# Kernel tuning notes

Hardware: AMD Instinct MI355X
Metric: run time of the kernel (lower is better)

## Reference

```python
import jax, jax.numpy as jnp
import numpy as np
from jax import lax

B, H, W = 8, 64, 64
D_IN, D_OUT, HEADS = 288, 576, 8
WIN, QS = 16, 2
MLP_H, BOT, NEXP = 4 * D_OUT, 32, 2
HEAD_DIM = D_OUT // HEADS


def _ln(x, g, b, eps=1e-6):
    m = jnp.mean(x, axis=-1, keepdims=True)
    v = jnp.var(x, axis=-1, keepdims=True)
    return (x - m) * lax.rsqrt(v + eps) * g + b


def _max_pool2(x):  # NHWC 2x2 max pool, stride 2
    return lax.reduce_window(x, -jnp.inf, lax.max, (1, 2, 2, 1), (1, 2, 2, 1), 'VALID')


def setup_inputs():
    key = jax.random.key(0)
    ks = iter(jax.random.split(key, 16))
    s = 0.02
    p = {}
    p['rgb'] = jax.random.normal(next(ks), (B, H, W, D_IN), jnp.float32)
    p['depth'] = jax.random.normal(next(ks), (B, H, W, D_IN), jnp.float32)
    p['norm1_g'] = jnp.ones((D_IN,), jnp.float32)
    p['norm1_b'] = jnp.zeros((D_IN,), jnp.float32)
    p['proj_w'] = jax.random.normal(next(ks), (D_IN, D_OUT), jnp.float32) * s
    p['proj_b'] = jnp.zeros((D_OUT,), jnp.float32)
    p['qkv_w'] = jax.random.normal(next(ks), (D_IN, 3 * D_OUT), jnp.float32) * s
    p['qkv_b'] = jnp.zeros((3 * D_OUT,), jnp.float32)
    p['attn_proj_w'] = jax.random.normal(next(ks), (D_OUT, D_OUT), jnp.float32) * s
    p['attn_proj_b'] = jnp.zeros((D_OUT,), jnp.float32)
    p['norm2_g'] = jnp.ones((D_OUT,), jnp.float32)
    p['norm2_b'] = jnp.zeros((D_OUT,), jnp.float32)
    p['mlp_w1'] = jax.random.normal(next(ks), (D_OUT, MLP_H), jnp.float32) * s
    p['mlp_b1'] = jnp.zeros((MLP_H,), jnp.float32)
    p['mlp_w2'] = jax.random.normal(next(ks), (MLP_H, D_OUT), jnp.float32) * s
    p['mlp_b2'] = jnp.zeros((D_OUT,), jnp.float32)
    # per-stream (rgb=0, depth=1) MoE adapters: 2 experts, bottleneck 32
    p['ad_gate_w'] = jax.random.normal(next(ks), (2, D_OUT, NEXP), jnp.float32) * s
    p['ad_gate_b'] = jnp.zeros((2, NEXP), jnp.float32)
    p['ad_down_w'] = jax.random.normal(next(ks), (2, NEXP, D_OUT, BOT), jnp.float32) * s
    p['ad_down_b'] = jnp.zeros((2, NEXP, BOT), jnp.float32)
    p['ad_up_w'] = jax.random.normal(next(ks), (2, NEXP, BOT, D_OUT), jnp.float32) * s
    p['ad_up_b'] = jnp.zeros((2, NEXP, D_OUT), jnp.float32)
    return p


def reference(rgb, depth, norm1_g, norm1_b, proj_w, proj_b, qkv_w, qkv_b,
              attn_proj_w, attn_proj_b, norm2_g, norm2_b,
              mlp_w1, mlp_b1, mlp_w2, mlp_b2,
              ad_gate_w, ad_gate_b, ad_down_w, ad_down_b, ad_up_w, ad_up_b):
    nW = H // WIN  # 4 windows per side (64 divisible by 16, no padding)
    w2 = WIN // QS  # pooled window side = 8

    def adapter(x, si):
        gate = jax.nn.softmax(x @ ad_gate_w[si] + ad_gate_b[si], axis=-1)  # [B,h,w,E]
        h = jax.nn.gelu(jnp.einsum('bhwd,edr->bhwer', x, ad_down_w[si]) + ad_down_b[si])
        y = jnp.einsum('bhwer,erd->bhwed', h, ad_up_w[si]) + ad_up_b[si]
        return 0.5 * jnp.sum(gate[..., None] * y, axis=-2)

    def stream(x, si):
        xn = _ln(x, norm1_g, norm1_b)
        # dim changes -> shortcut = do_pool(proj(norm1(x)))
        shortcut = _max_pool2(xn @ proj_w + proj_b)  # [B,32,32,576]
        xw = xn.reshape(B, nW, WIN, nW, WIN, D_IN).transpose(0, 1, 3, 2, 4, 5)
        xw = xw.reshape(B * nW * nW, WIN, WIN, D_IN)
        Bw = xw.shape[0]
        qkv = (xw.reshape(Bw, WIN * WIN, D_IN) @ qkv_w + qkv_b)
        qkv = qkv.reshape(Bw, WIN * WIN, 3, HEADS, HEAD_DIM)
        q, k, v = qkv[:, :, 0], qkv[:, :, 1], qkv[:, :, 2]
        # q-pool (2x2 max) inside each window
        q = _max_pool2(q.reshape(Bw, WIN, WIN, D_OUT)).reshape(Bw, w2 * w2, HEADS, HEAD_DIM)
        scale = 1.0 / np.sqrt(HEAD_DIM).astype(np.float32)
        attn = jax.nn.softmax(jnp.einsum('bqhd,bkhd->bhqk', q, k) * scale, axis=-1)
        o = jnp.einsum('bhqk,bkhd->bqhd', attn, v).reshape(Bw, w2, w2, D_OUT)
        o = o @ attn_proj_w + attn_proj_b
        # unpartition with pooled window size into 32x32
        o = o.reshape(B, nW, nW, w2, w2, D_OUT).transpose(0, 1, 3, 2, 4, 5)
        o = o.reshape(B, nW * w2, nW * w2, D_OUT)
        x = shortcut + o
        h = _ln(x, norm2_g, norm2_b)
        mlp = jax.nn.gelu(h @ mlp_w1 + mlp_b1) @ mlp_w2 + mlp_b2
        return x + mlp + adapter(x, si)

    return jnp.stack([stream(rgb, 0), stream(depth, 1)])  # [2,B,32,32,576]
```

## Files before the change

### kernel.cpp

```cpp
#include <hip/hip_runtime.h>
#include <cstdint>
#include <math.h>
#include <type_traits>

typedef __bf16 bf16_t;
typedef __bf16 bf16x8 __attribute__((ext_vector_type(8)));
typedef float f32x4 __attribute__((ext_vector_type(4)));
typedef uint32_t u32x4 __attribute__((ext_vector_type(4)));
typedef uint32_t u32x2 __attribute__((ext_vector_type(2)));

#define DI __device__ __forceinline__

DI float bflo(uint32_t u){ return __builtin_bit_cast(float, (uint32_t)(u << 16)); }
DI float bfhi(uint32_t u){ return __builtin_bit_cast(float, (uint32_t)(u & 0xffff0000u)); }
DI uint16_t f2bf(float f){ bf16_t h = (bf16_t)f; return __builtin_bit_cast(uint16_t, h); }
DI uint32_t pk2(float a, float b){ return (uint32_t)f2bf(a) | ((uint32_t)f2bf(b) << 16); }
DI float geluf(float x){
  float t = x * x;
  float p = fmaf(t, 0.0356774081f, 0.7978845608f);
  float e = __expf(-2.0f * x * p);
  return x * __builtin_amdgcn_rcpf(1.0f + e);
}

#if defined(__has_builtin)
#if __has_builtin(__builtin_amdgcn_global_load_lds)
#define USE_GLLDS 1
#endif
#endif

#if USE_GLLDS
DI void gload_lds16(const void* g, void* l){
  __builtin_amdgcn_global_load_lds((__attribute__((address_space(1))) void*)g,
                                   (__attribute__((address_space(3))) void*)l, 16, 0, 0);
}
#endif

__global__ __launch_bounds__(256) void wprep_k(
    const float* __restrict__ proj_w, const float* __restrict__ qkv_w,
    const float* __restrict__ ap_w, const float* __restrict__ w1,
    const float* __restrict__ proj_b, const float* __restrict__ qkv_b,
    uint16_t* __restrict__ pqT, uint16_t* __restrict__ kvT,
    uint16_t* __restrict__ aT, uint16_t* __restrict__ m1T, float* __restrict__ pqB)
{
  const int y = blockIdx.y;
  const int idx = blockIdx.x * 256 + threadIdx.x;
  if (y == 5){
    if (idx < 1152) pqB[idx] = (idx < 576) ? proj_b[idx] : qkv_b[idx - 576];
    return;
  }
  const float* W; uint16_t* Wt; int K, N, Np, ldw, c0;
  switch (y){
    case 0: W = proj_w; Wt = pqT;                      K = 288; N = 576;  Np = 576;  ldw = 576;  c0 = 0;   break;
    case 1: W = qkv_w;  Wt = pqT + (size_t)576 * 288;  K = 288; N = 576;  Np = 576;  ldw = 1728; c0 = 0;   break;
    case 2: W = qkv_w;  Wt = kvT;                      K = 288; N = 1152; Np = 1152; ldw = 1728; c0 = 576; break;
    case 3: W = ap_w;   Wt = aT;                       K = 576; N = 576;  Np = 640;  ldw = 576;  c0 = 0;   break;
    default:W = w1;     Wt = m1T;                      K = 576; N = 2304; Np = 2304; ldw = 2304; c0 = 0;   break;
  }
  if (idx >= Np * K) return;
  int n = idx / K, k = idx - n * K;
  float v = (n < N) ? W[(size_t)k * ldw + c0 + n] : 0.0f;
  Wt[idx] = f2bf(v);
}

__global__ __launch_bounds__(256) void mk_m2te_k(const float* __restrict__ w2,
    const float* __restrict__ uw, const float* __restrict__ ub, uint16_t* __restrict__ m2Te)
{
  int idx = blockIdx.x * 256 + threadIdx.x;
  if (idx >= 2 * 640 * 2400) return;
  int si = idx / (640 * 2400);
  int rem = idx - si * 640 * 2400;
  int n = rem / 2400, k = rem - n * 2400;
  float v = 0.0f;
  if (n < 576){
    if (k < 2304) v = w2[(size_t)k * 576 + n];
    else if (k < 2368){
      int e = (k - 2304) >> 5, r = (k - 2304) & 31;
      v = uw[((size_t)(si * 2 + e) * 32 + r) * 576 + n];
    } else if (k < 2370){
      v = ub[(size_t)(si * 2 + (k - 2368)) * 576 + n];
    }
  }
  m2Te[idx] = f2bf(v);
}

__global__ __launch_bounds__(256) void mk_adt_k(const float* __restrict__ dwn, const float* __restrict__ gw,
    const float* __restrict__ dbn, const float* __restrict__ gb,
    uint16_t* __restrict__ adT, float* __restrict__ adB)
{
  int idx = blockIdx.x * 256 + threadIdx.x;
  if (idx >= 2 * 128 * 576) return;
  int si = idx / (128 * 576);
  int rem = idx - si * 128 * 576;
  int n = rem / 576, k = rem - n * 576;
  float v = 0.0f;
  if (n < 64){
    int e = n >> 5, r = n & 31;
    v = dwn[((size_t)(si * 2 + e) * 576 + k) * 32 + r];
  } else if (n < 66){
    v = gw[(size_t)si * 1152 + k * 2 + (n - 64)];
  }
  adT[idx] = f2bf(v);
  if (k == 0){
    float bv = 0.0f;
    if (n < 64) bv = dbn[si * 64 + (n >> 5) * 32 + (n & 31)];
    else if (n < 66) bv = gb[si * 2 + (n - 64)];
    adB[si * 128 + n] = bv;
  }
}

template<typename TIN>
__global__ __launch_bounds__(256) void ln_k(const TIN* __restrict__ inA, const TIN* __restrict__ inB,
                                            const int rowsA, const int D,
                                            const float* __restrict__ g, const float* __restrict__ bb,
                                            uint16_t* __restrict__ outp)
{
  const int token = blockIdx.x * 4 + (threadIdx.x >> 6);
  const int lane = threadIdx.x & 63;
  const TIN* in = (token < rowsA) ? (inA + (size_t)token * D) : (inB + (size_t)(token - rowsA) * D);
  const int nf4 = D >> 2;
  f32x4 v[3];
  float s = 0.f, sq = 0.f;
#pragma unroll
  for (int i = 0; i < 3; ++i){
    const int c = lane + 64 * i;
    if (c < nf4){
      if constexpr (std::is_same<TIN, float>::value){
        v[i] = *(const f32x4*)(in + 4 * c);
      } else {
        u32x2 u = *(const u32x2*)((const uint16_t*)in + 4 * c);
        v[i][0] = bflo(u[0]); v[i][1] = bfhi(u[0]);
        v[i][2] = bflo(u[1]); v[i][3] = bfhi(u[1]);
      }
#pragma unroll
      for (int e = 0; e < 4; ++e){ s += v[i][e]; sq += v[i][e] * v[i][e]; }
    }
  }
#pragma unroll
  for (int off = 32; off; off >>= 1){
    s  += __shfl_xor(s, off);
    sq += __shfl_xor(sq, off);
  }
  const float mean = s / (float)D;
  const float var = sq / (float)D - mean * mean;
  const float inv = rsqrtf(var + 1e-6f);
  uint16_t* orow = outp + (size_t)token * D;
#pragma unroll
  for (int i = 0; i < 3; ++i){
    const int c = lane + 64 * i;
    if (c < nf4){
      float f0 = (v[i][0] - mean) * inv * g[4*c+0] + bb[4*c+0];
      float f1 = (v[i][1] - mean) * inv * g[4*c+1] + bb[4*c+1];
      float f2 = (v[i][2] - mean) * inv * g[4*c+2] + bb[4*c+2];
      float f3 = (v[i][3] - mean) * inv * g[4*c+3] + bb[4*c+3];
      u32x2 pk; pk[0] = pk2(f0, f1); pk[1] = pk2(f2, f3);
      *(u32x2*)(orow + 4 * c) = pk;
    }
  }
}

template<int BM, int KK>
DI void gemm_core(const uint16_t* __restrict__ A, const uint16_t* __restrict__ Bt,
                  char* smem, const int tid, f32x4 (*acc)[4])
{
  constexpr int MI = BM / 32;
  constexpr int ABUF = BM * 64;
  constexpr int nt = KK >> 5;
  char* A0 = smem;
  char* A1 = smem + ABUF;
  char* B0 = smem + 2 * ABUF;
  char* B1 = smem + 2 * ABUF + 8192;
  const int lane = tid & 63;
  const int wid = tid >> 6;
  const int wm = (wid >> 1) * (BM / 2);
  const int wn = (wid & 1) * 64;
  const int r15 = lane & 15, kh = lane >> 4;
  const int rA0 = tid >> 2, c16 = tid & 3;
  const int kS = ((c16 ^ ((rA0 >> 1) & 3)) << 3);

  auto stage = [&](char* Ad, char* Bd, int t){
    const uint16_t* ga0 = A + (size_t)rA0 * KK + t * 32 + kS;
    const uint16_t* gb0 = Bt + (size_t)rA0 * KK + t * 32 + kS;
    const uint16_t* gb1 = Bt + (size_t)(rA0 + 64) * KK + t * 32 + kS;
#if USE_GLLDS
    gload_lds16(ga0, Ad + tid * 16);
    gload_lds16(gb0, Bd + tid * 16);
    gload_lds16(gb1, Bd + tid * 16 + 4096);
    if constexpr (BM == 128){
      const uint16_t* ga1 = A + (size_t)(rA0 + 64) * KK + t * 32 + kS;
      gload_lds16(ga1, Ad + tid * 16 + 4096);
    }
#else
    *(u32x4*)(Ad + tid * 16)        = *(const u32x4*)ga0;
    *(u32x4*)(Bd + tid * 16)        = *(const u32x4*)gb0;
    *(u32x4*)(Bd + tid * 16 + 4096) = *(const u32x4*)gb1;
    if constexpr (BM == 128){
      const uint16_t* ga1 = A + (size_t)(rA0 + 64) * KK + t * 32 + kS;
      *(u32x4*)(Ad + tid * 16 + 4096) = *(const u32x4*)ga1;
    }
#endif
  };

  stage(A0, B0, 0);
  __syncthreads();
  for (int t = 0; t < nt; ++t){
    char* Ac = (t & 1) ? A1 : A0;
    char* Bc = (t & 1) ? B1 : B0;
    if (t + 1 < nt) stage((t & 1) ? A0 : A1, (t & 1) ? B0 : B1, t + 1);
    bf16x8 af[MI], bfv[4];
#pragma unroll
    for (int i = 0; i < MI; ++i){
      int rowA = wm + i * 16 + r15;
      af[i] = *(const bf16x8*)(Ac + rowA * 64 + ((kh ^ ((rowA >> 1) & 3)) << 4));
    }
#pragma unroll
    for (int j = 0; j < 4; ++j){
      int rowB = wn + j * 16 + r15;
      bfv[j] = *(const bf16x8*)(Bc + rowB * 64 + ((kh ^ ((rowB >> 1) & 3)) << 4));
    }
#pragma unroll
    for (int i = 0; i < MI; ++i)
#pragma unroll
      for (int j = 0; j < 4; ++j)
        acc[i][j] = __builtin_amdgcn_mfma_f32_16x16x32_bf16(af[i], bfv[j], acc[i][j], 0, 0, 0);
    __syncthreads();
  }
}

__global__ __launch_bounds__(256) void gemm_pkv_k(
    const uint16_t* __restrict__ xn, const uint16_t* __restrict__ pqT, const uint16_t* __restrict__ kvT,
    const float* __restrict__ pqB, const float* __restrict__ kvB,
    uint16_t* __restrict__ sc, uint16_t* __restrict__ qp,
    uint16_t* __restrict__ kb, uint16_t* __restrict__ vt)
{
  __shared__ __align__(16) char smem[34816];
  const int tid = threadIdx.x;
  const int m0 = blockIdx.x * 128;
  const int y = blockIdx.y;
  const bool pool = (y < 9);
  const int n0 = pool ? y * 128 : (y - 9) * 128;
  const uint16_t* Bt = (pool ? pqT : kvT) + (size_t)n0 * 288;
  f32x4 acc[4][4] = {};
  gemm_core<128, 288>(xn + (size_t)m0 * 288, Bt, smem, tid, acc);

  const int lane = tid & 63, wid = tid >> 6;
  const int wm = (wid >> 1) * 64, wn = (wid & 1) * 64;
  const int r15 = lane & 15, kh = lane >> 4;

  if (pool){
    uint16_t* Cp = (uint16_t*)smem;
#pragma unroll
    for (int i = 0; i < 4; ++i)
#pragma unroll
      for (int j = 0; j < 4; ++j)
#pragma unroll
        for (int tt = 0; tt < 4; ++tt){
          int rr2 = wm + i * 16 + kh * 4 + tt;
          int cc = wn + j * 16 + r15;
          Cp[rr2 * 136 + cc] = f2bf(acc[i][j][tt]);
        }
    __syncthreads();
    const int orow0 = m0 >> 2;
#pragma unroll
    for (int e2 = 0; e2 < 16; ++e2){
      int idx = tid + 256 * e2;
      int X = idx >> 7, c = idx & 127;
      int gn = n0 + c;
      float v0 = bflo(Cp[(2 * X) * 136 + c]);
      float v1 = bflo(Cp[(2 * X + 1) * 136 + c]);
      float v2 = bflo(Cp[(64 + 2 * X) * 136 + c]);
      float v3 = bflo(Cp[(65 + 2 * X) * 136 + c]);
      float v = fmaxf(fmaxf(v0, v1), fmaxf(v2, v3)) + pqB[gn];
      if (gn < 576)
        sc[(size_t)(orow0 + X) * 576 + gn] = f2bf(v);
      else
        qp[(size_t)(orow0 + X) * 576 + (gn - 576)] = f2bf(v);
    }
  } else {
    int coln[4]; float bcol[4];
#pragma unroll
    for (int j = 0; j < 4; ++j){
      coln[j] = n0 + wn + j * 16 + r15;
      bcol[j] = kvB[coln[j]];
    }
#pragma unroll
    for (int i = 0; i < 4; ++i)
#pragma unroll
      for (int tt = 0; tt < 4; ++tt){
        const int gm = m0 + wm + i * 16 + kh * 4 + tt;
#pragma unroll
        for (int j = 0; j < 4; ++j){
          float v = acc[i][j][tt] + bcol[j];
          int n = coln[j];
          if (n < 576){
            kb[(size_t)gm * 576 + n] = f2bf(v);
          } else {
            int d = n - 576;
            int hh = d / 72, dd = d - hh * 72;
            int bimg = gm >> 12, yy = (gm >> 6) & 63, xx = gm & 63;
            int w = bimg * 16 + (yy >> 4) * 4 + (xx >> 4);
            int kl = (yy & 15) * 16 + (xx & 15);
            vt[((size_t)(w * 8 + hh) * 80 + dd) * 256 + kl] = f2bf(v);
          }
        }
      }
  }
}

__global__ __launch_bounds__(256) void gemm_add1_k(
    const uint16_t* __restrict__ ob, const uint16_t* __restrict__ aT, const float* __restrict__ bias,
    const uint16_t* __restrict__ sc, uint16_t* __restrict__ x2b)
{
  __shared__ __align__(16) char smem[32768];
  const int tid = threadIdx.x;
  const int m0 = blockIdx.x * 128;
  const int n0 = blockIdx.y * 128;
  f32x4 acc[4][4] = {};
  gemm_core<128, 576>(ob + (size_t)m0 * 576, aT + (size_t)n0 * 576, smem, tid, acc);

  const int lane = tid & 63, wid = tid >> 6;
  const int wm = (wid >> 1) * 64, wn = (wid & 1) * 64;
  const int r15 = lane & 15, kh = lane >> 4;
  int coln[4]; float bcol[4];
#pragma unroll
  for (int j = 0; j < 4; ++j){
    coln[j] = n0 + wn + j * 16 + r15;
    bcol[j] = (coln[j] < 576) ? bias[coln[j]] : 0.0f;
  }
#pragma unroll
  for (int i = 0; i < 4; ++i)
#pragma unroll
    for (int tt = 0; tt < 4; ++tt){
      const int gm = m0 + wm + i * 16 + kh * 4 + tt;
      const size_t ro = (size_t)gm * 576;
#pragma unroll
      for (int j = 0; j < 4; ++j){
        if (coln[j] < 576){
          float v = acc[i][j][tt] + bcol[j] + bflo(sc[ro + coln[j]]);
          x2b[ro + coln[j]] = f2bf(v);
        }
      }
    }
}

__global__ __launch_bounds__(256) void gemm_upad_k(
    const uint16_t* __restrict__ hb, const uint16_t* __restrict__ x2b,
    const uint16_t* __restrict__ m1T, const uint16_t* __restrict__ adT,
    const float* __restrict__ b1, const float* __restrict__ adB,
    uint16_t* __restrict__ mlpA)
{
  __shared__ __align__(16) char smem[32768];
  const int tid = threadIdx.x;
  const int m0 = blockIdx.x * 128;
  const int y = blockIdx.y;
  const bool up = (y < 18);
  const int si = m0 >> 13;
  const int n0 = up ? y * 128 : 0;
  const uint16_t* A = (up ? hb : x2b) + (size_t)m0 * 576;
  const uint16_t* Bt = up ? (m1T + (size_t)n0 * 576) : (adT + (size_t)si * 128 * 576);
  f32x4 acc[4][4] = {};
  gemm_core<128, 576>(A, Bt, smem, tid, acc);

  const int lane = tid & 63, wid = tid >> 6;
  const int wm = (wid >> 1) * 64, wn = (wid & 1) * 64;
  const int r15 = lane & 15, kh = lane >> 4;

  if (up){
#pragma unroll
    for (int i = 0; i < 4; ++i)
#pragma unroll
      for (int tt = 0; tt < 4; ++tt){
        const int gm = m0 + wm + i * 16 + kh * 4 + tt;
#pragma unroll
        for (int j = 0; j < 4; ++j){
          int c = n0 + wn + j * 16 + r15;
          float v = acc[i][j][tt] + b1[c];
          mlpA[(size_t)gm * 2400 + c] = f2bf(geluf(v));
        }
      }
  } else {
    const float* adBp = adB + si * 128;
    float* gl = (float*)smem;
#pragma unroll
    for (int i = 0; i < 4; ++i)
#pragma unroll
      for (int j = 0; j < 4; ++j){
        int c = wn + j * 16 + r15;
        if (c == 64 || c == 65){
#pragma unroll
          for (int tt = 0; tt < 4; ++tt){
            int rr2 = wm + i * 16 + kh * 4 + tt;
            gl[rr2 * 2 + (c - 64)] = acc[i][j][tt] + adBp[c];
          }
        }
      }
    __syncthreads();
#pragma unroll
    for (int i = 0; i < 4; ++i)
#pragma unroll
      for (int tt = 0; tt < 4; ++tt){
        int rr2 = wm + i * 16 + kh * 4 + tt;
        int gm = m0 + rr2;
        float l0 = gl[rr2 * 2], l1 = gl[rr2 * 2 + 1];
        float mx = fmaxf(l0, l1);
        float e0 = __expf(l0 - mx), e1 = __expf(l1 - mx);
        float inv = 0.5f / (e0 + e1);
#pragma unroll
        for (int j = 0; j < 4; ++j){
          int c = wn + j * 16 + r15;
          if (c < 96){
            float val;
            if (c < 64){
              float g = ((c >> 5) == 0 ? e0 : e1) * inv;
              val = g * geluf(acc[i][j][tt] + adBp[c]);
            } else if (c == 64) val = e0 * inv;
            else if (c == 65) val = e1 * inv;
            else val = 0.0f;
            mlpA[(size_t)gm * 2400 + 2304 + c] = f2bf(val);
          }
        }
      }
  }
}

__global__ __launch_bounds__(256) void gemm_addf_k(
    const uint16_t* __restrict__ mlpA, const uint16_t* __restrict__ m2Te, const float* __restrict__ bias,
    const uint16_t* __restrict__ x2b, float* __restrict__ outf)
{
  __shared__ __align__(16) char smem[32768];
  const int tid = threadIdx.x;
  const int m0 = blockIdx.x * 128;
  const int n0 = blockIdx.y * 128;
  const int si = m0 >> 13;
  f32x4 acc[4][4] = {};
  gemm_core<128, 2400>(mlpA + (size_t)m0 * 2400, m2Te + (size_t)si * 640 * 2400 + (size_t)n0 * 2400,
                       smem, tid, acc);

  const int lane = tid & 63, wid = tid >> 6;
  const int wm = (wid >> 1) * 64, wn = (wid & 1) * 64;
  const int r15 = lane & 15, kh = lane >> 4;
  int coln[4]; float bcol[4];
#pragma unroll
  for (int j = 0; j < 4; ++j){
    coln[j] = n0 + wn + j * 16 + r15;
    bcol[j] = (coln[j] < 576) ? bias[coln[j]] : 0.0f;
  }
#pragma unroll
  for (int i = 0; i < 4; ++i)
#pragma unroll
    for (int tt = 0; tt < 4; ++tt){
      const int gm = m0 + wm + i * 16 + kh * 4 + tt;
      const size_t ro = (size_t)gm * 576;
#pragma unroll
      for (int j = 0; j < 4; ++j){
        if (coln[j] < 576){
          float v = acc[i][j][tt] + bcol[j] + bflo(x2b[ro + coln[j]]);
          outf[ro + coln[j]] = v;
        }
      }
    }
}

__global__ __launch_bounds__(128) void attn_mfma_k(
    const uint16_t* __restrict__ qp,
    const uint16_t* __restrict__ kb,
    const uint16_t* __restrict__ vt,
    uint16_t* __restrict__ o)
{
  __shared__ float comb[64][88];
  const int tid = threadIdx.x;
  const int wave = tid >> 6;
  const int lane = tid & 63;
  const int r15 = lane & 15;
  const int kh = lane >> 4;
  const int bid = blockIdx.x;
  const int h = bid & 7;
  const int w = bid >> 3;
  const int b = w >> 4;
  const int wy = (w >> 2) & 3;
  const int wx = w & 3;

  const u32x4 ZU = {0, 0, 0, 0};
  const bf16x8 Z8 = __builtin_bit_cast(bf16x8, ZU);
  const float scale = 0.11785113019775793f;

  bf16x8 qf[4][3];
  int qrow[4];
#pragma unroll
  for (int j = 0; j < 4; ++j){
    int q = j * 16 + r15;
    int y = wy * 8 + (q >> 3), x = wx * 8 + (q & 7);
    qrow[j] = b * 1024 + y * 32 + x;
    const uint16_t* qpr = qp + (size_t)qrow[j] * 576 + h * 72;
    qf[j][0] = *(const bf16x8*)(qpr + kh * 8);
    qf[j][1] = *(const bf16x8*)(qpr + 32 + kh * 8);
    qf[j][2] = (kh == 0) ? *(const bf16x8*)(qpr + 64) : Z8;
  }

  float m[4], l[4];
#pragma unroll
  for (int j = 0; j < 4; ++j){ m[j] = -INFINITY; l[j] = 0.0f; }
  f32x4 acco[5][4] = {};
  const size_t vtbase = (size_t)(w * 8 + h) * 80 * 256;

#pragma unroll
  for (int t2 = 0; t2 < 2; ++t2){
    const int t = wave * 2 + t2;
    f32x4 accs[4][4] = {};
#pragma unroll
    for (int i = 0; i < 4; ++i){
      const uint16_t* kr = kb + (size_t)(b * 4096 + (wy * 16 + t * 4 + i) * 64 + wx * 16 + r15) * 576 + h * 72;
      bf16x8 kf0 = *(const bf16x8*)(kr + kh * 8);
      bf16x8 kf1 = *(const bf16x8*)(kr + 32 + kh * 8);
      bf16x8 kf2 = (kh == 0) ? *(const bf16x8*)(kr + 64) : Z8;
#pragma unroll
      for (int j = 0; j < 4; ++j){
        accs[i][j] = __builtin_amdgcn_mfma_f32_16x16x32_bf16(kf0, qf[j][0], accs[i][j], 0, 0, 0);
        accs[i][j] = __builtin_amdgcn_mfma_f32_16x16x32_bf16(kf1, qf[j][1], accs[i][j], 0, 0, 0);
        accs[i][j] = __builtin_amdgcn_mfma_f32_16x16x32_bf16(kf2, qf[j][2], accs[i][j], 0, 0, 0);
      }
    }
#pragma unroll
    for (int j = 0; j < 4; ++j){
      float mx = -INFINITY;
#pragma unroll
      for (int i = 0; i < 4; ++i)
#pragma unroll
        for (int tt = 0; tt < 4; ++tt){
          float sv = accs[i][j][tt] * scale;
          accs[i][j][tt] = sv;
          mx = fmaxf(mx, sv);
        }
      mx = fmaxf(mx, __shfl_xor(mx, 16));
      mx = fmaxf(mx, __shfl_xor(mx, 32));
      float nm = fmaxf(m[j], mx);
      float f = __expf(m[j] - nm);
      m[j] = nm;
      l[j] *= f;
#pragma unroll
      for (int i2 = 0; i2 < 5; ++i2) acco[i2][j] *= f;
      float ls = 0.0f;
#pragma unroll
      for (int i = 0; i < 4; ++i)
#pragma unroll
        for (int tt = 0; tt < 4; ++tt){
          float p = __expf(accs[i][j][tt] - nm);
          accs[i][j][tt] = p;
          ls += p;
        }
      ls += __shfl_xor(ls, 16);
      ls += __shfl_xor(ls, 32);
      l[j] += ls;
    }
    uint32_t pw[4][4][2];
#pragma unroll
    for (int i = 0; i < 4; ++i)
#pragma unroll
      for (int j = 0; j < 4; ++j){
        pw[i][j][0] = pk2(accs[i][j][0], accs[i][j][1]);
        pw[i][j][1] = pk2(accs[i][j][2], accs[i][j][3]);
      }
#pragma unroll
    for (int ks = 0; ks < 2; ++ks){
      bf16x8 pb[4];
#pragma unroll
      for (int j = 0; j < 4; ++j){
        u32x4 u = {pw[2 * ks][j][0], pw[2 * ks][j][1], pw[2 * ks + 1][j][0], pw[2 * ks + 1][j][1]};
        pb[j] = __builtin_bit_cast(bf16x8, u);
      }
#pragma unroll
      for (int i2 = 0; i2 < 5; ++i2){
        const uint16_t* vr = vt + vtbase + (size_t)(i2 * 16 + r15) * 256 + t * 64 + ks * 32 + kh * 4;
        u32x2 lo = *(const u32x2*)(vr);
        u32x2 hi = *(const u32x2*)(vr + 16);
        u32x4 av = {lo[0], lo[1], hi[0], hi[1]};
        bf16x8 va = __builtin_bit_cast(bf16x8, av);
#pragma unroll
        for (int j = 0; j < 4; ++j)
          acco[i2][j] = __builtin_amdgcn_mfma_f32_16x16x32_bf16(va, pb[j], acco[i2][j], 0, 0, 0);
      }
    }
  }

  if (wave == 1){
#pragma unroll
    for (int j = 0; j < 4; ++j){ comb[lane][j] = m[j]; comb[lane][4 + j] = l[j]; }
#pragma unroll
    for (int i2 = 0; i2 < 5; ++i2)
#pragma unroll
      for (int j = 0; j < 4; ++j)
#pragma unroll
        for (int tt = 0; tt < 4; ++tt)
          comb[lane][8 + (i2 * 4 + j) * 4 + tt] = acco[i2][j][tt];
  }
  __syncthreads();
  if (wave == 0){
    float fs0[4], fs1[4];
#pragma unroll
    for (int j = 0; j < 4; ++j){
      float m1v = comb[lane][j], l1v = comb[lane][4 + j];
      float nm = fmaxf(m[j], m1v);
      fs0[j] = __expf(m[j] - nm);
      fs1[j] = __expf(m1v - nm);
      l[j] = l[j] * fs0[j] + l1v * fs1[j];
    }
#pragma unroll
    for (int j = 0; j < 4; ++j){
      float inv = 1.0f / l[j];
      uint16_t* orow = o + (size_t)qrow[j] * 576 + h * 72;
#pragma unroll
      for (int i2 = 0; i2 < 5; ++i2){
        const int d0 = i2 * 16 + kh * 4;
        if (d0 < 72){
          float ov[4];
#pragma unroll
          for (int tt = 0; tt < 4; ++tt)
            ov[tt] = (acco[i2][j][tt] * fs0[j] + comb[lane][8 + (i2 * 4 + j) * 4 + tt] * fs1[j]) * inv;
          u32x2 pk; pk[0] = pk2(ov[0], ov[1]); pk[1] = pk2(ov[2], ov[3]);
          *(u32x2*)(orow + d0) = pk;
        }
      }
    }
  }
}

extern "C" void kernel_launch(void* const* d_in, const int* in_sizes, int n_in,
                              void* d_out, int out_size, void* d_ws, size_t ws_size,
                              hipStream_t stream)
{
  (void)in_sizes; (void)n_in; (void)out_size; (void)ws_size;
  const float* rgb    = (const float*)d_in[0];
  const float* depth  = (const float*)d_in[1];
  const float* n1g    = (const float*)d_in[2];
  const float* n1b    = (const float*)d_in[3];
  const float* proj_w = (const float*)d_in[4];
  const float* proj_b = (const float*)d_in[5];
  const float* qkv_w  = (const float*)d_in[6];
  const float* qkv_b  = (const float*)d_in[7];
  const float* ap_w   = (const float*)d_in[8];
  const float* ap_b   = (const float*)d_in[9];
  const float* n2g    = (const float*)d_in[10];
  const float* n2b    = (const float*)d_in[11];
  const float* w1     = (const float*)d_in[12];
  const float* b1     = (const float*)d_in[13];
  const float* w2     = (const float*)d_in[14];
  const float* b2     = (const float*)d_in[15];
  const float* gw     = (const float*)d_in[16];
  const float* gb     = (const float*)d_in[17];
  const float* dwn    = (const float*)d_in[18];
  const float* dbn    = (const float*)d_in[19];
  const float* uw     = (const float*)d_in[20];
  const float* ub     = (const float*)d_in[21];

  char* ws = (char*)d_ws;
  size_t off = 0;
  auto alloc = [&](size_t bytes){ size_t o = off; off += (bytes + 255) & ~(size_t)255; return o; };

  uint16_t* pqT   = (uint16_t*)(ws + alloc((size_t)1152 * 288 * 2));
  float*    pqB   = (float*)(ws + alloc((size_t)1152 * 4));
  uint16_t* kvT   = (uint16_t*)(ws + alloc((size_t)1152 * 288 * 2));
  uint16_t* aT    = (uint16_t*)(ws + alloc((size_t)640 * 576 * 2));
  uint16_t* m1T   = (uint16_t*)(ws + alloc((size_t)2304 * 576 * 2));
  uint16_t* m2Te  = (uint16_t*)(ws + alloc((size_t)2 * 640 * 2400 * 2));
  uint16_t* adT   = (uint16_t*)(ws + alloc((size_t)2 * 128 * 576 * 2));
  float*    adB   = (float*)(ws + alloc((size_t)2 * 128 * 4));
  uint16_t* xn2  = (uint16_t*)(ws + alloc((size_t)65536 * 288 * 2));
  uint16_t* sc2  = (uint16_t*)(ws + alloc((size_t)16384 * 576 * 2));
  size_t oQP = alloc((size_t)16384 * 576 * 2);
  uint16_t* qp2  = (uint16_t*)(ws + oQP);
  uint16_t* x2b  = (uint16_t*)(ws + oQP);
  uint16_t* kb   = (uint16_t*)(ws + alloc((size_t)32768 * 576 * 2));
  size_t oVT = alloc((size_t)16384 * 2400 * 2);
  uint16_t* vt   = (uint16_t*)(ws + oVT);
  uint16_t* mlpA = (uint16_t*)(ws + oVT);
  size_t oOB = alloc((size_t)16384 * 576 * 2);
  uint16_t* ob2  = (uint16_t*)(ws + oOB);
  uint16_t* hb2  = (uint16_t*)(ws + oOB);

  wprep_k<<<dim3(5184, 6), 256, 0, stream>>>(proj_w, qkv_w, ap_w, w1, proj_b, qkv_b,
                                             pqT, kvT, aT, m1T, pqB);
  mk_m2te_k<<<(2 * 640 * 2400 + 255) / 256, 256, 0, stream>>>(w2, uw, ub, m2Te);
  mk_adt_k<<<(2 * 128 * 576 + 255) / 256, 256, 0, stream>>>(dwn, gw, dbn, gb, adT, adB);

  ln_k<float><<<16384, 256, 0, stream>>>(rgb, depth, 32768, 288, n1g, n1b, xn2);

  for (int si = 0; si < 2; ++si){
    const size_t half = (size_t)si * 8192 * 576;

    gemm_pkv_k<<<dim3(256, 18), 256, 0, stream>>>(xn2 + (size_t)si * 32768 * 288, pqT, kvT,
                                                  pqB, qkv_b + 576,
                                                  sc2 + half, qp2 + half, kb, vt);

    attn_mfma_k<<<1024, 128, 0, stream>>>(qp2 + half, kb, vt, ob2 + half);
  }

  gemm_add1_k<<<dim3(128, 5), 256, 0, stream>>>(ob2, aT, ap_b, sc2, x2b);

  ln_k<uint16_t><<<4096, 256, 0, stream>>>(x2b, x2b, 16384, 576, n2g, n2b, hb2);

  gemm_upad_k<<<dim3(128, 19), 256, 0, stream>>>(hb2, x2b, m1T, adT, b1, adB, mlpA);

  gemm_addf_k<<<dim3(128, 5), 256, 0, stream>>>(mlpA, m2Te, b2, x2b, (float*)d_out);
}
```

Baseline: 556.7 us.

## Merge weight-prep kernels and swap GEMM grid order for A-tile reuse

Folds the two separate weight-conversion kernels (m2Te and adapter transposes) into the main wprep kernel as extra grid rows, cutting two launches. It also swaps the grid dimensions of all four GEMM kernels, so the N-tile index runs fastest and consecutive blocks share the same M-row A tile. The intent is better L2 reuse of the large activation operands, with less launch overhead as a side benefit. The merged prep grid is much larger (12000x8), and most blocks in the smaller rows exit immediately.

```diff
diff --git a/kernel.cpp b/kernel.cpp
--- a/kernel.cpp
+++ b/kernel.cpp
@@ -39,13 +39,56 @@
     const float* __restrict__ proj_w, const float* __restrict__ qkv_w,
     const float* __restrict__ ap_w, const float* __restrict__ w1,
     const float* __restrict__ proj_b, const float* __restrict__ qkv_b,
+    const float* __restrict__ w2, const float* __restrict__ uw, const float* __restrict__ ub,
+    const float* __restrict__ dwn, const float* __restrict__ gw,
+    const float* __restrict__ dbn, const float* __restrict__ gb,
     uint16_t* __restrict__ pqT, uint16_t* __restrict__ kvT,
-    uint16_t* __restrict__ aT, uint16_t* __restrict__ m1T, float* __restrict__ pqB)
+    uint16_t* __restrict__ aT, uint16_t* __restrict__ m1T, float* __restrict__ pqB,
+    uint16_t* __restrict__ m2Te, uint16_t* __restrict__ adT, float* __restrict__ adB)
 {
   const int y = blockIdx.y;
   const int idx = blockIdx.x * 256 + threadIdx.x;
   if (y == 5){
     if (idx < 1152) pqB[idx] = (idx < 576) ? proj_b[idx] : qkv_b[idx - 576];
+    return;
+  }
+  if (y == 6){
+    if (idx >= 2 * 640 * 2400) return;
+    int si = idx / (640 * 2400);
+    int rem = idx - si * 640 * 2400;
+    int n = rem / 2400, k = rem - n * 2400;
+    float v = 0.0f;
+    if (n < 576){
+      if (k < 2304) v = w2[(size_t)k * 576 + n];
+      else if (k < 2368){
+        int e = (k - 2304) >> 5, r = (k - 2304) & 31;
+        v = uw[((size_t)(si * 2 + e) * 32 + r) * 576 + n];
+      } else if (k < 2370){
+        v = ub[(size_t)(si * 2 + (k - 2368)) * 576 + n];
+      }
+    }
+    m2Te[idx] = f2bf(v);
+    return;
+  }
+  if (y == 7){
+    if (idx >= 2 * 128 * 576) return;
+    int si = idx / (128 * 576);
+    int rem = idx - si * 128 * 576;
+    int n = rem / 576, k = rem - n * 576;
+    float v = 0.0f;
+    if (n < 64){
+      int e = n >> 5, r = n & 31;
+      v = dwn[((size_t)(si * 2 + e) * 576 + k) * 32 + r];
+    } else if (n < 66){
+      v = gw[(size_t)si * 1152 + k * 2 + (n - 64)];
+    }
+    adT[idx] = f2bf(v);
+    if (k == 0){
+      float bv = 0.0f;
+      if (n < 64) bv = dbn[si * 64 + (n >> 5) * 32 + (n & 31)];
+      else if (n < 66) bv = gb[si * 2 + (n - 64)];
+      adB[si * 128 + n] = bv;
+    }
     return;
   }
   const float* W; uint16_t* Wt; int K, N, Np, ldw, c0;
@@ -60,52 +103,6 @@
   int n = idx / K, k = idx - n * K;
   float v = (n < N) ? W[(size_t)k * ldw + c0 + n] : 0.0f;
   Wt[idx] = f2bf(v);
-}
-
-__global__ __launch_bounds__(256) void mk_m2te_k(const float* __restrict__ w2,
-    const float* __restrict__ uw, const float* __restrict__ ub, uint16_t* __restrict__ m2Te)
-{
-  int idx = blockIdx.x * 256 + threadIdx.x;
-  if (idx >= 2 * 640 * 2400) return;
-  int si = idx / (640 * 2400);
-  int rem = idx - si * 640 * 2400;
-  int n = rem / 2400, k = rem - n * 2400;
-  float v = 0.0f;
-  if (n < 576){
-    if (k < 2304) v = w2[(size_t)k * 576 + n];
-    else if (k < 2368){
-      int e = (k - 2304) >> 5, r = (k - 2304) & 31;
-      v = uw[((size_t)(si * 2 + e) * 32 + r) * 576 + n];
-    } else if (k < 2370){
-      v = ub[(size_t)(si * 2 + (k - 2368)) * 576 + n];
-    }
-  }
-  m2Te[idx] = f2bf(v);
-}
-
-__global__ __launch_bounds__(256) void mk_adt_k(const float* __restrict__ dwn, const float* __restrict__ gw,
-    const float* __restrict__ dbn, const float* __restrict__ gb,
-    uint16_t* __restrict__ adT, float* __restrict__ adB)
-{
-  int idx = blockIdx.x * 256 + threadIdx.x;
-  if (idx >= 2 * 128 * 576) return;
-  int si = idx / (128 * 576);
-  int rem = idx - si * 128 * 576;
-  int n = rem / 576, k = rem - n * 576;
-  float v = 0.0f;
-  if (n < 64){
-    int e = n >> 5, r = n & 31;
-    v = dwn[((size_t)(si * 2 + e) * 576 + k) * 32 + r];
-  } else if (n < 66){
-    v = gw[(size_t)si * 1152 + k * 2 + (n - 64)];
-  }
-  adT[idx] = f2bf(v);
-  if (k == 0){
-    float bv = 0.0f;
-    if (n < 64) bv = dbn[si * 64 + (n >> 5) * 32 + (n & 31)];
-    else if (n < 66) bv = gb[si * 2 + (n - 64)];
-    adB[si * 128 + n] = bv;
-  }
 }
 
 template<typename TIN>
@@ -234,8 +231,8 @@
 {
   __shared__ __align__(16) char smem[34816];
   const int tid = threadIdx.x;
-  const int m0 = blockIdx.x * 128;
-  const int y = blockIdx.y;
+  const int m0 = blockIdx.y * 128;
+  const int y = blockIdx.x;
   const bool pool = (y < 9);
   const int n0 = pool ? y * 128 : (y - 9) * 128;
   const uint16_t* Bt = (pool ? pqT : kvT) + (size_t)n0 * 288;
@@ -312,8 +309,8 @@
 {
   __shared__ __align__(16) char smem[32768];
   const int tid = threadIdx.x;
-  const int m0 = blockIdx.x * 128;
-  const int n0 = blockIdx.y * 128;
+  const int m0 = blockIdx.y * 128;
+  const int n0 = blockIdx.x * 128;
   f32x4 acc[4][4] = {};
   gemm_core<128, 576>(ob + (size_t)m0 * 576, aT + (size_t)n0 * 576, smem, tid, acc);
 
@@ -350,8 +347,8 @@
 {
   __shared__ __align__(16) char smem[32768];
   const int tid = threadIdx.x;
-  const int m0 = blockIdx.x * 128;
-  const int y = blockIdx.y;
+  const int m0 = blockIdx.y * 128;
+  const int y = blockIdx.x;
   const bool up = (y < 18);
   const int si = m0 >> 13;
   const int n0 = up ? y * 128 : 0;
@@ -428,8 +425,8 @@
 {
   __shared__ __align__(16) char smem[32768];
   const int tid = threadIdx.x;
-  const int m0 = blockIdx.x * 128;
-  const int n0 = blockIdx.y * 128;
+  const int m0 = blockIdx.y * 128;
+  const int n0 = blockIdx.x * 128;
   const int si = m0 >> 13;
   f32x4 acc[4][4] = {};
   gemm_core<128, 2400>(mlpA + (size_t)m0 * 2400, m2Te + (size_t)si * 640 * 2400 + (size_t)n0 * 2400,
@@ -676,28 +673,27 @@
   uint16_t* ob2  = (uint16_t*)(ws + oOB);
   uint16_t* hb2  = (uint16_t*)(ws + oOB);
 
-  wprep_k<<<dim3(5184, 6), 256, 0, stream>>>(proj_w, qkv_w, ap_w, w1, proj_b, qkv_b,
-                                             pqT, kvT, aT, m1T, pqB);
-  mk_m2te_k<<<(2 * 640 * 2400 + 255) / 256, 256, 0, stream>>>(w2, uw, ub, m2Te);
-  mk_adt_k<<<(2 * 128 * 576 + 255) / 256, 256, 0, stream>>>(dwn, gw, dbn, gb, adT, adB);
+  wprep_k<<<dim3(12000, 8), 256, 0, stream>>>(proj_w, qkv_w, ap_w, w1, proj_b, qkv_b,
+                                              w2, uw, ub, dwn, gw, dbn, gb,
+                                              pqT, kvT, aT, m1T, pqB, m2Te, adT, adB);
 
   ln_k<float><<<16384, 256, 0, stream>>>(rgb, depth, 32768, 288, n1g, n1b, xn2);
 
   for (int si = 0; si < 2; ++si){
     const size_t half = (size_t)si * 8192 * 576;
 
-    gemm_pkv_k<<<dim3(256, 18), 256, 0, stream>>>(xn2 + (size_t)si * 32768 * 288, pqT, kvT,
+    gemm_pkv_k<<<dim3(18, 256), 256, 0, stream>>>(xn2 + (size_t)si * 32768 * 288, pqT, kvT,
                                                   pqB, qkv_b + 576,
                                                   sc2 + half, qp2 + half, kb, vt);
 
     attn_mfma_k<<<1024, 128, 0, stream>>>(qp2 + half, kb, vt, ob2 + half);
   }
 
-  gemm_add1_k<<<dim3(128, 5), 256, 0, stream>>>(ob2, aT, ap_b, sc2, x2b);
+  gemm_add1_k<<<dim3(5, 128), 256, 0, stream>>>(ob2, aT, ap_b, sc2, x2b);
 
   ln_k<uint16_t><<<4096, 256, 0, stream>>>(x2b, x2b, 16384, 576, n2g, n2b, hb2);
 
-  gemm_upad_k<<<dim3(128, 19), 256, 0, stream>>>(hb2, x2b, m1T, adT, b1, adB, mlpA);
-
-  gemm_addf_k<<<dim3(128, 5), 256, 0, stream>>>(mlpA, m2Te, b2, x2b, (float*)d_out);
-}
+  gemm_upad_k<<<dim3(19, 128), 256, 0, stream>>>(hb2, x2b, m1T, adT, b1, adB, mlpA);
+
+  gemm_addf_k<<<dim3(5, 128), 256, 0, stream>>>(mlpA, m2Te, b2, x2b, (float*)d_out);
+}
```

After: 593.6 us. 6.6% more time.
